# Optimization experiments

Hardware: AMD Instinct MI355X
Metric: run time of the kernel (lower is better)

## Reference

```python
import jax, jax.numpy as jnp
import numpy as np

HEADS = 8
DIM_HEAD = 64
SCALE = DIM_HEAD ** -0.5


def setup_inputs() -> dict:
    key = jax.random.key(0)
    ks = jax.random.split(key, 7)
    b, p, n, dim = 4, 8, 512, 512
    inner = HEADS * DIM_HEAD
    std = dim ** -0.5
    return {
        "q_in": jax.random.normal(ks[0], (b, p, n, dim), jnp.float32),
        "kv_in": jax.random.normal(ks[1], (b, p, n, dim), jnp.float32),
        "Wq": jax.random.normal(ks[2], (dim, inner), jnp.float32) * std,
        "Wk": jax.random.normal(ks[3], (dim, inner), jnp.float32) * std,
        "Wv": jax.random.normal(ks[4], (dim, inner), jnp.float32) * std,
        "Wo": jax.random.normal(ks[5], (inner, dim), jnp.float32) * std,
        "bo": jnp.zeros((dim,), jnp.float32),
    }


def _split_heads(x):
    # [b, p, n, h*d] -> [b, h, p, n, d]
    b, p, n, hd = x.shape
    return x.reshape(b, p, n, HEADS, DIM_HEAD).transpose(0, 3, 1, 2, 4)


def reference(q_in, kv_in, Wq, Wk, Wv, Wo, bo):
    q = _split_heads(q_in @ Wq)
    k = _split_heads(kv_in @ Wk)
    v = _split_heads(kv_in @ Wv)
    dots = jnp.einsum('bhpid,bhpjd->bhpij', q, k) * SCALE
    attn = jax.nn.softmax(dots, axis=-1)
    out = jnp.einsum('bhpij,bhpjd->bhpid', attn, v)
    # [b, h, p, n, d] -> [b, p, n, h*d]
    b, h, p, n, d = out.shape
    out = out.transpose(0, 2, 3, 1, 4).reshape(b, p, n, h * d)
    return out @ Wo + bo
```

## Files before the change

### kernel.cpp

```cpp
#include <hip/hip_runtime.h>

typedef unsigned short u16;
typedef u16  u16x8 __attribute__((ext_vector_type(8)));
typedef u16  u16x4 __attribute__((ext_vector_type(4)));
typedef float f32x4 __attribute__((ext_vector_type(4)));
typedef __bf16 bf16x8 __attribute__((ext_vector_type(8)));

#define SEQ   512
#define DIM   512
#define DHEAD 64
#define M_ROWS 16384

#define AS1 __attribute__((address_space(1)))
#define AS3 __attribute__((address_space(3)))
#define GLL16(gp, lp) __builtin_amdgcn_global_load_lds((const AS1 void*)(gp), (AS3 void*)(lp), 16, 0, 0)

__device__ __forceinline__ u16 f2b(float f) {
  unsigned int x = __builtin_bit_cast(unsigned int, f);
  return (u16)((x + 0x7fffu + ((x >> 16) & 1u)) >> 16);
}

__global__ __launch_bounds__(256) void convert_in(const float* __restrict__ q,
                                                  const float* __restrict__ kv,
                                                  u16* __restrict__ qb,
                                                  u16* __restrict__ kvb) {
  const float* src = blockIdx.y ? kv : q;
  u16* dst = blockIdx.y ? kvb : qb;
  size_t i = ((size_t)blockIdx.x * 256 + threadIdx.x) * 8;
  float4 a = *reinterpret_cast<const float4*>(&src[i]);
  float4 b = *reinterpret_cast<const float4*>(&src[i + 4]);
  u16x8 o;
  o[0] = f2b(a.x); o[1] = f2b(a.y); o[2] = f2b(a.z); o[3] = f2b(a.w);
  o[4] = f2b(b.x); o[5] = f2b(b.y); o[6] = f2b(b.z); o[7] = f2b(b.w);
  *reinterpret_cast<u16x8*>(&dst[i]) = o;
}

__global__ __launch_bounds__(256) void wtrans(const float* __restrict__ Wq,
                                              const float* __restrict__ Wk,
                                              const float* __restrict__ Wv,
                                              const float* __restrict__ Wo,
                                              u16* __restrict__ out) {
  __shared__ float tile[32][33];
  const int tid = threadIdx.x;
  const int tx = tid & 31, ty = tid >> 5;
  const int z = blockIdx.z;
  const float* W = (z == 0) ? Wq : (z == 1) ? Wk : (z == 2) ? Wv : Wo;
  const int n0 = blockIdx.x * 32;
  const int k0 = blockIdx.y * 32;
#pragma unroll
  for (int i = 0; i < 4; i++) {
    int r = ty + i * 8;
    tile[r][tx] = W[(k0 + r) * DIM + n0 + tx];
  }
  __syncthreads();
  u16* o = out + (size_t)z * DIM * DIM;
#pragma unroll
  for (int i = 0; i < 4; i++) {
    int r = ty + i * 8;
    o[(n0 + r) * DIM + k0 + tx] = f2b(tile[tx][r]);
  }
}

__global__ __launch_bounds__(256) void gemm_qkv(const u16* __restrict__ Qin,
                                                const u16* __restrict__ KVin,
                                                const u16* __restrict__ Wqt,
                                                const u16* __restrict__ Wkt,
                                                const u16* __restrict__ Wvt,
                                                u16* __restrict__ Qb,
                                                u16* __restrict__ Kb,
                                                u16* __restrict__ Vt) {
  __shared__ __attribute__((aligned(16))) u16 As[128 * 32];
  __shared__ __attribute__((aligned(16))) u16 Bs[128 * 32];
  const int tid = threadIdx.x;
  const int lane = tid & 63;
  const int w = tid >> 6;
  const int l15 = lane & 15;
  const int quad = lane >> 4;
  const int z = blockIdx.z;
  const int wr = (w >> 1) * 64, wc = (w & 1) * 64;
  const int srow = lane >> 2;
  const int scol = (lane & 3) * 8;

  int gm, gn;
  const u16 *A, *B;
  if (z < 2) {
    gm = blockIdx.y * 128; gn = blockIdx.x * 128;
    A = z ? KVin : Qin;  B = z ? Wkt : Wqt;
  } else {
    gm = blockIdx.x * 128; gn = blockIdx.y * 128;
    A = Wvt; B = KVin;
  }

  f32x4 acc[4][4] = {};

  for (int k0 = 0; k0 < DIM; k0 += 32) {
    __syncthreads();
#pragma unroll
    for (int i = 0; i < 2; i++) {
      int r0 = w * 32 + i * 16;
      GLL16(&A[(size_t)(gm + r0 + srow) * DIM + k0 + scol], &As[r0 * 32]);
      GLL16(&B[(size_t)(gn + r0 + srow) * DIM + k0 + scol], &Bs[r0 * 32]);
    }
    __syncthreads();

    bf16x8 af[4], bfr[4];
#pragma unroll
    for (int mt = 0; mt < 4; mt++)
      af[mt] = *reinterpret_cast<const bf16x8*>(&As[(wr + mt * 16 + l15) * 32 + quad * 8]);
#pragma unroll
    for (int nt = 0; nt < 4; nt++)
      bfr[nt] = *reinterpret_cast<const bf16x8*>(&Bs[(wc + nt * 16 + l15) * 32 + quad * 8]);
#pragma unroll
    for (int mt = 0; mt < 4; mt++)
#pragma unroll
      for (int nt = 0; nt < 4; nt++)
        acc[mt][nt] = __builtin_amdgcn_mfma_f32_16x16x32_bf16(af[mt], bfr[nt], acc[mt][nt], 0, 0, 0);
  }

  if (z < 2) {
    u16* C = (z == 0) ? Qb : Kb;
#pragma unroll
    for (int mt = 0; mt < 4; mt++)
#pragma unroll
      for (int nt = 0; nt < 4; nt++)
#pragma unroll
        for (int r = 0; r < 4; r++)
          C[(gm + wr + mt * 16 + quad * 4 + r) * DIM + gn + wc + nt * 16 + l15] = f2b(acc[mt][nt][r]);
  } else {
#pragma unroll
    for (int mt = 0; mt < 4; mt++)
#pragma unroll
      for (int nt = 0; nt < 4; nt++)
#pragma unroll
        for (int r = 0; r < 4; r++)
          Vt[(size_t)(gm + wr + mt * 16 + quad * 4 + r) * M_ROWS + gn + wc + nt * 16 + l15] = f2b(acc[mt][nt][r]);
  }
}

__global__ __launch_bounds__(256) void attn(const u16* __restrict__ Qb,
                                            const u16* __restrict__ Kb,
                                            const u16* __restrict__ Vtg,
                                            u16* __restrict__ Ob) {
  __shared__ __attribute__((aligned(16))) u16 Ks[2 * 128 * 32];
  __shared__ __attribute__((aligned(16))) u16 Vs[4 * 64 * 32];
  __shared__ __attribute__((aligned(16))) u16 Pq[4][16 * 136];

  const int tid = threadIdx.x;
  const int lane = tid & 63;
  const int w = tid >> 6;
  const int l15 = lane & 15;
  const int quad = lane >> 4;
  const int srow = lane >> 2;
  const int scol = (lane & 3) * 8;

  const int bid = blockIdx.x;
  const int qt = bid & 3;
  const int bhp = bid >> 2;
  const int h = bhp & 7;
  const int bp = bhp >> 3;
  const int qrow0 = bp * SEQ + qt * 128;
  const int col0 = h * DHEAD;

  bf16x8 qf[2][2];
#pragma unroll
  for (int g = 0; g < 2; g++)
#pragma unroll
    for (int kd = 0; kd < 2; kd++)
      qf[g][kd] = *reinterpret_cast<const bf16x8*>(
          &Qb[(size_t)(qrow0 + w * 32 + g * 16 + l15) * DIM + col0 + kd * 32 + quad * 8]);

  float m_[2] = {-1e30f, -1e30f}, l_[2] = {0.0f, 0.0f};
  f32x4 o[2][4] = {};

  for (int j = 0; j < 4; j++) {
    __syncthreads();
    const int krow0 = bp * SEQ + j * 128;
#pragma unroll
    for (int i = 0; i < 4; i++) {
      int t = w * 4 + i;
      int plane = t & 1, chunk = t >> 1;
      GLL16(&Kb[(size_t)(krow0 + chunk * 16 + srow) * DIM + col0 + plane * 32 + scol],
            &Ks[plane * 4096 + chunk * 512]);
    }
#pragma unroll
    for (int i = 0; i < 4; i++) {
      int t = w * 4 + i;
      int plane = t & 3, chunk = t >> 2;
      GLL16(&Vtg[(size_t)(col0 + chunk * 16 + srow) * M_ROWS + krow0 + plane * 32 + scol],
            &Vs[plane * 2048 + chunk * 512]);
    }
    __syncthreads();

#pragma unroll
    for (int g = 0; g < 2; g++) {
      f32x4 st[8];
#pragma unroll
      for (int ct = 0; ct < 8; ct++) {
        f32x4 z = {};
#pragma unroll
        for (int kd = 0; kd < 2; kd++) {
          bf16x8 kf = *reinterpret_cast<const bf16x8*>(&Ks[kd * 4096 + (ct * 16 + l15) * 32 + quad * 8]);
          z = __builtin_amdgcn_mfma_f32_16x16x32_bf16(kf, qf[g][kd], z, 0, 0, 0);
        }
        st[ct] = z * 0.125f;
      }

      float pm = -1e30f;
#pragma unroll
      for (int ct = 0; ct < 8; ct++)
#pragma unroll
        for (int r = 0; r < 4; r++) pm = fmaxf(pm, st[ct][r]);
      pm = fmaxf(pm, __shfl_xor(pm, 16));
      pm = fmaxf(pm, __shfl_xor(pm, 32));
      float mn = fmaxf(m_[g], pm);
      float alpha = __expf(m_[g] - mn);
      m_[g] = mn;
      float rs = 0.0f;
#pragma unroll
      for (int ct = 0; ct < 8; ct++)
#pragma unroll
        for (int r = 0; r < 4; r++) {
          float pv = __expf(st[ct][r] - mn);
          st[ct][r] = pv;
          rs += pv;
        }
      rs += __shfl_xor(rs, 16);
      rs += __shfl_xor(rs, 32);
      l_[g] = l_[g] * alpha + rs;
#pragma unroll
      for (int r = 0; r < 4; r++) {
        float ar = __shfl(alpha, quad * 4 + r);
#pragma unroll
        for (int nt = 0; nt < 4; nt++) o[g][nt][r] *= ar;
      }

#pragma unroll
      for (int ct = 0; ct < 8; ct++) {
        u16x4 pk;
#pragma unroll
        for (int e = 0; e < 4; e++) pk[e] = f2b(st[ct][e]);
        *reinterpret_cast<u16x4*>(&Pq[w][l15 * 136 + ct * 16 + quad * 4]) = pk;
      }
      __threadfence_block();

#pragma unroll
      for (int c2 = 0; c2 < 4; c2++) {
        bf16x8 af = *reinterpret_cast<const bf16x8*>(&Pq[w][l15 * 136 + c2 * 32 + quad * 8]);
#pragma unroll
        for (int nt = 0; nt < 4; nt++) {
          bf16x8 bv = *reinterpret_cast<const bf16x8*>(&Vs[c2 * 2048 + (nt * 16 + l15) * 32 + quad * 8]);
          o[g][nt] = __builtin_amdgcn_mfma_f32_16x16x32_bf16(af, bv, o[g][nt], 0, 0, 0);
        }
      }
      __threadfence_block();
    }
  }

#pragma unroll
  for (int g = 0; g < 2; g++) {
    float inv = 1.0f / l_[g];
#pragma unroll
    for (int r = 0; r < 4; r++) {
      float lr = __shfl(inv, quad * 4 + r);
      int row = qrow0 + w * 32 + g * 16 + quad * 4 + r;
#pragma unroll
      for (int nt = 0; nt < 4; nt++)
        Ob[(size_t)row * DIM + col0 + nt * 16 + l15] = f2b(o[g][nt][r] * lr);
    }
  }
}

__global__ __launch_bounds__(256) void gemm_out(const u16* __restrict__ Ab,
                                                const u16* __restrict__ Bt,
                                                const float* __restrict__ bias,
                                                float* __restrict__ C) {
  __shared__ __attribute__((aligned(16))) u16 As[128 * 32];
  __shared__ __attribute__((aligned(16))) u16 Bs[128 * 32];
  const int tid = threadIdx.x;
  const int lane = tid & 63;
  const int w = tid >> 6;
  const int l15 = lane & 15;
  const int quad = lane >> 4;
  const int gm = blockIdx.y * 128;
  const int gn = blockIdx.x * 128;
  const int wr = (w >> 1) * 64, wc = (w & 1) * 64;
  const int srow = lane >> 2;
  const int scol = (lane & 3) * 8;

  f32x4 acc[4][4] = {};

  for (int k0 = 0; k0 < DIM; k0 += 32) {
    __syncthreads();
#pragma unroll
    for (int i = 0; i < 2; i++) {
      int r0 = w * 32 + i * 16;
      GLL16(&Ab[(size_t)(gm + r0 + srow) * DIM + k0 + scol], &As[r0 * 32]);
      GLL16(&Bt[(size_t)(gn + r0 + srow) * DIM + k0 + scol], &Bs[r0 * 32]);
    }
    __syncthreads();

    bf16x8 af[4], bfr[4];
#pragma unroll
    for (int mt = 0; mt < 4; mt++)
      af[mt] = *reinterpret_cast<const bf16x8*>(&As[(wr + mt * 16 + l15) * 32 + quad * 8]);
#pragma unroll
    for (int nt = 0; nt < 4; nt++)
      bfr[nt] = *reinterpret_cast<const bf16x8*>(&Bs[(wc + nt * 16 + l15) * 32 + quad * 8]);
#pragma unroll
    for (int mt = 0; mt < 4; mt++)
#pragma unroll
      for (int nt = 0; nt < 4; nt++)
        acc[mt][nt] = __builtin_amdgcn_mfma_f32_16x16x32_bf16(af[mt], bfr[nt], acc[mt][nt], 0, 0, 0);
  }

#pragma unroll
  for (int mt = 0; mt < 4; mt++)
#pragma unroll
    for (int nt = 0; nt < 4; nt++) {
      float bcol = bias[gn + wc + nt * 16 + l15];
#pragma unroll
      for (int r = 0; r < 4; r++)
        C[(gm + wr + mt * 16 + quad * 4 + r) * DIM + gn + wc + nt * 16 + l15] = acc[mt][nt][r] + bcol;
    }
}

extern "C" void kernel_launch(void* const* d_in, const int* in_sizes, int n_in,
                              void* d_out, int out_size, void* d_ws, size_t ws_size,
                              hipStream_t stream) {
  const float* q_in  = (const float*)d_in[0];
  const float* kv_in = (const float*)d_in[1];
  const float* Wq    = (const float*)d_in[2];
  const float* Wk    = (const float*)d_in[3];
  const float* Wv    = (const float*)d_in[4];
  const float* Wo    = (const float*)d_in[5];
  const float* bo    = (const float*)d_in[6];
  float* out = (float*)d_out;

  u16* ws = (u16*)d_ws;
  u16* Wqt = ws;
  u16* Wkt = ws + 262144;
  u16* Wvt = ws + 524288;
  u16* Wot = ws + 786432;
  u16* Qb  = ws + 1048576;
  u16* Kb  = Qb + (size_t)M_ROWS * DIM;
  u16* Vtg = Kb + (size_t)M_ROWS * DIM;
  u16* Ob  = Vtg + (size_t)M_ROWS * DIM;
  u16* Qin_b  = (u16*)d_out;
  u16* KVin_b = Qin_b + (size_t)M_ROWS * DIM;

  convert_in<<<dim3(4096, 2), 256, 0, stream>>>(q_in, kv_in, Qin_b, KVin_b);
  wtrans<<<dim3(16, 16, 4), 256, 0, stream>>>(Wq, Wk, Wv, Wo, ws);
  gemm_qkv<<<dim3(4, 128, 3), 256, 0, stream>>>(Qin_b, KVin_b, Wqt, Wkt, Wvt, Qb, Kb, Vtg);
  attn<<<dim3(1024), 256, 0, stream>>>(Qb, Kb, Vtg, Ob);
  gemm_out<<<dim3(4, 128), 256, 0, stream>>>(Ob, Wot, bo, out);
}
```

Baseline: 233.5 us.

## Enlarge QKV GEMM tile to 256x128 and merge input prep kernels

Combines the activation bf16 conversion and weight transpose into a single prep kernel to cut one launch. The QKV projection GEMM now uses 256x128 block tiles, with each wave computing 128x64 outputs, so each B tile load is reused more. In exchange, accumulator register use doubles, launch bounds request 2 blocks per CU, and the grid halves, which may lower occupancy and wave balance.

```diff
diff --git a/kernel.cpp b/kernel.cpp
--- a/kernel.cpp
+++ b/kernel.cpp
@@ -1,6 +1,7 @@
 #include <hip/hip_runtime.h>
 
 typedef unsigned short u16;
+typedef unsigned int   u32;
 typedef u16  u16x8 __attribute__((ext_vector_type(8)));
 typedef u16  u16x4 __attribute__((ext_vector_type(4)));
 typedef float f32x4 __attribute__((ext_vector_type(4)));
@@ -16,60 +17,64 @@
 #define GLL16(gp, lp) __builtin_amdgcn_global_load_lds((const AS1 void*)(gp), (AS3 void*)(lp), 16, 0, 0)
 
 __device__ __forceinline__ u16 f2b(float f) {
-  unsigned int x = __builtin_bit_cast(unsigned int, f);
+  u32 x = __builtin_bit_cast(u32, f);
   return (u16)((x + 0x7fffu + ((x >> 16) & 1u)) >> 16);
 }
 
-__global__ __launch_bounds__(256) void convert_in(const float* __restrict__ q,
-                                                  const float* __restrict__ kv,
-                                                  u16* __restrict__ qb,
-                                                  u16* __restrict__ kvb) {
-  const float* src = blockIdx.y ? kv : q;
-  u16* dst = blockIdx.y ? kvb : qb;
-  size_t i = ((size_t)blockIdx.x * 256 + threadIdx.x) * 8;
-  float4 a = *reinterpret_cast<const float4*>(&src[i]);
-  float4 b = *reinterpret_cast<const float4*>(&src[i + 4]);
-  u16x8 o;
-  o[0] = f2b(a.x); o[1] = f2b(a.y); o[2] = f2b(a.z); o[3] = f2b(a.w);
-  o[4] = f2b(b.x); o[5] = f2b(b.y); o[6] = f2b(b.z); o[7] = f2b(b.w);
-  *reinterpret_cast<u16x8*>(&dst[i]) = o;
-}
-
-__global__ __launch_bounds__(256) void wtrans(const float* __restrict__ Wq,
-                                              const float* __restrict__ Wk,
-                                              const float* __restrict__ Wv,
-                                              const float* __restrict__ Wo,
-                                              u16* __restrict__ out) {
+__global__ __launch_bounds__(256) void prep(const float* __restrict__ q,
+                                            const float* __restrict__ kv,
+                                            const float* __restrict__ Wq,
+                                            const float* __restrict__ Wk,
+                                            const float* __restrict__ Wv,
+                                            const float* __restrict__ Wo,
+                                            u16* __restrict__ qb,
+                                            u16* __restrict__ kvb,
+                                            u16* __restrict__ wout) {
   __shared__ float tile[32][33];
-  const int tid = threadIdx.x;
-  const int tx = tid & 31, ty = tid >> 5;
-  const int z = blockIdx.z;
-  const float* W = (z == 0) ? Wq : (z == 1) ? Wk : (z == 2) ? Wv : Wo;
-  const int n0 = blockIdx.x * 32;
-  const int k0 = blockIdx.y * 32;
-#pragma unroll
-  for (int i = 0; i < 4; i++) {
-    int r = ty + i * 8;
-    tile[r][tx] = W[(k0 + r) * DIM + n0 + tx];
-  }
-  __syncthreads();
-  u16* o = out + (size_t)z * DIM * DIM;
-#pragma unroll
-  for (int i = 0; i < 4; i++) {
-    int r = ty + i * 8;
-    o[(n0 + r) * DIM + k0 + tx] = f2b(tile[tx][r]);
-  }
-}
-
-__global__ __launch_bounds__(256) void gemm_qkv(const u16* __restrict__ Qin,
-                                                const u16* __restrict__ KVin,
-                                                const u16* __restrict__ Wqt,
-                                                const u16* __restrict__ Wkt,
-                                                const u16* __restrict__ Wvt,
-                                                u16* __restrict__ Qb,
-                                                u16* __restrict__ Kb,
-                                                u16* __restrict__ Vt) {
-  __shared__ __attribute__((aligned(16))) u16 As[128 * 32];
+  const int bid = blockIdx.x;
+  if (bid < 8192) {
+    const float* src = (bid >= 4096) ? kv : q;
+    u16* dst = (bid >= 4096) ? kvb : qb;
+    size_t i = ((size_t)(bid & 4095) * 256 + threadIdx.x) * 8;
+    float4 a = *reinterpret_cast<const float4*>(&src[i]);
+    float4 b = *reinterpret_cast<const float4*>(&src[i + 4]);
+    u16x8 o;
+    o[0] = f2b(a.x); o[1] = f2b(a.y); o[2] = f2b(a.z); o[3] = f2b(a.w);
+    o[4] = f2b(b.x); o[5] = f2b(b.y); o[6] = f2b(b.z); o[7] = f2b(b.w);
+    *reinterpret_cast<u16x8*>(&dst[i]) = o;
+  } else {
+    const int rem = bid - 8192;
+    const int z = rem >> 8;
+    const int t = rem & 255;
+    const int n0 = (t & 15) * 32;
+    const int k0 = (t >> 4) * 32;
+    const int tid = threadIdx.x;
+    const int tx = tid & 31, ty = tid >> 5;
+    const float* W = (z == 0) ? Wq : (z == 1) ? Wk : (z == 2) ? Wv : Wo;
+#pragma unroll
+    for (int i = 0; i < 4; i++) {
+      int r = ty + i * 8;
+      tile[r][tx] = W[(k0 + r) * DIM + n0 + tx];
+    }
+    __syncthreads();
+    u16* o = wout + (size_t)z * DIM * DIM;
+#pragma unroll
+    for (int i = 0; i < 4; i++) {
+      int r = ty + i * 8;
+      o[(n0 + r) * DIM + k0 + tx] = f2b(tile[tx][r]);
+    }
+  }
+}
+
+__global__ __launch_bounds__(256, 2) void gemm_qkv(const u16* __restrict__ Qin,
+                                                   const u16* __restrict__ KVin,
+                                                   const u16* __restrict__ Wqt,
+                                                   const u16* __restrict__ Wkt,
+                                                   const u16* __restrict__ Wvt,
+                                                   u16* __restrict__ Qb,
+                                                   u16* __restrict__ Kb,
+                                                   u16* __restrict__ Vt) {
+  __shared__ __attribute__((aligned(16))) u16 As[256 * 32];
   __shared__ __attribute__((aligned(16))) u16 Bs[128 * 32];
   const int tid = threadIdx.x;
   const int lane = tid & 63;
@@ -77,41 +82,46 @@
   const int l15 = lane & 15;
   const int quad = lane >> 4;
   const int z = blockIdx.z;
-  const int wr = (w >> 1) * 64, wc = (w & 1) * 64;
+  const int bid = blockIdx.x;
+  const int wr = (w >> 1) * 128, wc = (w & 1) * 64;
   const int srow = lane >> 2;
   const int scol = (lane & 3) * 8;
 
   int gm, gn;
   const u16 *A, *B;
   if (z < 2) {
-    gm = blockIdx.y * 128; gn = blockIdx.x * 128;
+    gm = (bid >> 2) * 256;  gn = (bid & 3) * 128;
     A = z ? KVin : Qin;  B = z ? Wkt : Wqt;
   } else {
-    gm = blockIdx.x * 128; gn = blockIdx.y * 128;
+    gm = (bid & 1) * 256;   gn = (bid >> 1) * 128;
     A = Wvt; B = KVin;
   }
 
-  f32x4 acc[4][4] = {};
+  f32x4 acc[8][4] = {};
 
   for (int k0 = 0; k0 < DIM; k0 += 32) {
     __syncthreads();
+#pragma unroll
+    for (int i = 0; i < 4; i++) {
+      int r0 = w * 64 + i * 16;
+      GLL16(&A[(size_t)(gm + r0 + srow) * DIM + k0 + scol], &As[r0 * 32]);
+    }
 #pragma unroll
     for (int i = 0; i < 2; i++) {
       int r0 = w * 32 + i * 16;
-      GLL16(&A[(size_t)(gm + r0 + srow) * DIM + k0 + scol], &As[r0 * 32]);
       GLL16(&B[(size_t)(gn + r0 + srow) * DIM + k0 + scol], &Bs[r0 * 32]);
     }
     __syncthreads();
 
-    bf16x8 af[4], bfr[4];
-#pragma unroll
-    for (int mt = 0; mt < 4; mt++)
+    bf16x8 af[8], bfr[4];
+#pragma unroll
+    for (int mt = 0; mt < 8; mt++)
       af[mt] = *reinterpret_cast<const bf16x8*>(&As[(wr + mt * 16 + l15) * 32 + quad * 8]);
 #pragma unroll
     for (int nt = 0; nt < 4; nt++)
       bfr[nt] = *reinterpret_cast<const bf16x8*>(&Bs[(wc + nt * 16 + l15) * 32 + quad * 8]);
 #pragma unroll
-    for (int mt = 0; mt < 4; mt++)
+    for (int mt = 0; mt < 8; mt++)
 #pragma unroll
       for (int nt = 0; nt < 4; nt++)
         acc[mt][nt] = __builtin_amdgcn_mfma_f32_16x16x32_bf16(af[mt], bfr[nt], acc[mt][nt], 0, 0, 0);
@@ -120,15 +130,15 @@
   if (z < 2) {
     u16* C = (z == 0) ? Qb : Kb;
 #pragma unroll
-    for (int mt = 0; mt < 4; mt++)
+    for (int mt = 0; mt < 8; mt++)
 #pragma unroll
       for (int nt = 0; nt < 4; nt++)
 #pragma unroll
         for (int r = 0; r < 4; r++)
-          C[(gm + wr + mt * 16 + quad * 4 + r) * DIM + gn + wc + nt * 16 + l15] = f2b(acc[mt][nt][r]);
+          C[(size_t)(gm + wr + mt * 16 + quad * 4 + r) * DIM + gn + wc + nt * 16 + l15] = f2b(acc[mt][nt][r]);
   } else {
 #pragma unroll
-    for (int mt = 0; mt < 4; mt++)
+    for (int mt = 0; mt < 8; mt++)
 #pragma unroll
       for (int nt = 0; nt < 4; nt++)
 #pragma unroll
@@ -320,7 +330,7 @@
       float bcol = bias[gn + wc + nt * 16 + l15];
 #pragma unroll
       for (int r = 0; r < 4; r++)
-        C[(gm + wr + mt * 16 + quad * 4 + r) * DIM + gn + wc + nt * 16 + l15] = acc[mt][nt][r] + bcol;
+        C[(size_t)(gm + wr + mt * 16 + quad * 4 + r) * DIM + gn + wc + nt * 16 + l15] = acc[mt][nt][r] + bcol;
     }
 }
 
@@ -348,9 +358,8 @@
   u16* Qin_b  = (u16*)d_out;
   u16* KVin_b = Qin_b + (size_t)M_ROWS * DIM;
 
-  convert_in<<<dim3(4096, 2), 256, 0, stream>>>(q_in, kv_in, Qin_b, KVin_b);
-  wtrans<<<dim3(16, 16, 4), 256, 0, stream>>>(Wq, Wk, Wv, Wo, ws);
-  gemm_qkv<<<dim3(4, 128, 3), 256, 0, stream>>>(Qin_b, KVin_b, Wqt, Wkt, Wvt, Qb, Kb, Vtg);
+  prep<<<dim3(9216), 256, 0, stream>>>(q_in, kv_in, Wq, Wk, Wv, Wo, Qin_b, KVin_b, ws);
+  gemm_qkv<<<dim3(256, 1, 3), 256, 0, stream>>>(Qin_b, KVin_b, Wqt, Wkt, Wvt, Qb, Kb, Vtg);
   attn<<<dim3(1024), 256, 0, stream>>>(Qb, Kb, Vtg, Ob);
   gemm_out<<<dim3(4, 128), 256, 0, stream>>>(Ob, Wot, bo, out);
 }
```

Result: no change. 229.2 us (-1.9%).
